# Kernel optimization log

Hardware: AMD Instinct MI355X
Metric: run time of the kernel (lower is better)

Reference implementation:

```python
import jax, jax.numpy as jnp
import numpy as np

# TFMBSLinear forward: quantize input and weight to ternary {-1,0,1} via sign,
# compute out = sign(x) @ sign(W)^T (what the ternary fabric T-GEMV kernel
# computes, with zero-skip), then add float bias. The base-3 byte packing is a
# transport encoding only; the math is the ternary matmul.

def setup_inputs() -> dict:
    key = jax.random.key(0)
    k1, k2, k3 = jax.random.split(key, 3)
    B, IN, OUT = 8192, 2048, 2048
    x = jax.random.normal(k1, (B, IN), dtype=jnp.float32)
    # kaiming-uniform-ish init; only sign matters for the fabric kernel
    weight = jax.random.normal(k2, (OUT, IN), dtype=jnp.float32)
    fan_in_bound = 1.0 / np.sqrt(IN)
    bias = jax.random.uniform(k3, (OUT,), dtype=jnp.float32,
                              minval=-fan_in_bound, maxval=fan_in_bound)
    return {"input": x, "weight": weight, "bias": bias}

def reference(input, weight, bias):
    x_t = jnp.sign(input)    # ternary activations [B, IN]
    w_t = jnp.sign(weight)   # ternary weights     [OUT, IN]
    out = jnp.einsum('bi,oi->bo', x_t, w_t)  # T-GEMV accumulation, fp32
    return out + bias
```

## Files before the change

### kernel.cpp

```cpp
#include <hip/hip_runtime.h>


typedef int   intx4    __attribute__((ext_vector_type(4)));
typedef int   intx8    __attribute__((ext_vector_type(8)));
typedef float floatx16 __attribute__((ext_vector_type(16)));

static constexpr int M = 8192;
static constexpr int N = 2048;
static constexpr int K = 2048;
static constexpr int KB = K / 2;
static constexpr int BM = 128, BN = 128;

__device__ __forceinline__ unsigned nib(float v) {
    unsigned u = __float_as_uint(v);
    return (v != 0.0f) ? (0x2u | ((u >> 28) & 0x8u)) : 0u;
}

__device__ __forceinline__ unsigned pack8(const float4& a, const float4& b) {
    return  nib(a.x)        | (nib(a.y) << 4)  | (nib(a.z) << 8)  | (nib(a.w) << 12)
         | (nib(b.x) << 16) | (nib(b.y) << 20) | (nib(b.z) << 24) | (nib(b.w) << 28);
}

__global__ __launch_bounds__(256) void quant_tile(
    const float* __restrict__ x, const float* __restrict__ w,
    uint4* __restrict__ qx, uint4* __restrict__ qw, int nx, int ntot)
{
    int g = blockIdx.x * 256 + threadIdx.x;
    if (g >= ntot) return;
    const float* src; uint4* dst; int gg;
    if (g < nx) { gg = g; src = x; dst = qx; }
    else        { gg = g - nx; src = w; dst = qw; }
    const int r = gg & 31, h = (gg >> 5) & 1, c = (gg >> 6) & 31, s = gg >> 11;
    const int m = s * 32 + r;
    const float4* p = (const float4*)(src + (size_t)m * K + (c * 2 + h) * 32);
    uint4 o;
    o.x = pack8(p[0], p[1]);
    o.y = pack8(p[2], p[3]);
    o.z = pack8(p[4], p[5]);
    o.w = pack8(p[6], p[7]);
    dst[gg] = o;
}

__device__ __forceinline__ intx8 ext4(intx4 v) {
    return __builtin_shufflevector(v, v, 0, 1, 2, 3, -1, -1, -1, -1);
}

__global__ __launch_bounds__(256, 3) void tgemm_fp4(
    const char* __restrict__ A,
    const char* __restrict__ B,
    const float* __restrict__ bias,
    float* __restrict__ C)
{
    __shared__ char sA[16384];
    __shared__ char sB[16384];

    const int tid  = threadIdx.x;
    const int wave = tid >> 6;
    const int lane = tid & 63;
    const int l32  = lane & 31;
    const int half = lane >> 5;

    const int bm = blockIdx.x * BM;
    const int bn = blockIdx.y * BN;

    const char* gA = A + ((size_t)(bm >> 5) + wave) * 32768 + lane * 16;
    const char* gB = B + ((size_t)(bn >> 5) + wave) * 32768 + lane * 16;
    char* lA = sA + wave * 4096;
    char* lB = sB + wave * 4096;

    const int wm = (wave & 1) * 64;
    const int wn = (wave >> 1) * 64;

    const int aoff = (wm >> 5) * 4096 + lane * 16;
    const int boff = (wn >> 5) * 4096 + lane * 16;

    floatx16 acc[2][2] = {};

    for (int it = 0; it < 8; ++it) {
        const char* ga = gA + it * 4096;
        const char* gb = gB + it * 4096;
        #pragma unroll
        for (int t = 0; t < 4; ++t) {
            __builtin_amdgcn_global_load_lds(
                (const __attribute__((address_space(1))) void*)(ga + t * 1024),
                (__attribute__((address_space(3))) void*)(lA + t * 1024), 16, 0, 0);
            __builtin_amdgcn_global_load_lds(
                (const __attribute__((address_space(1))) void*)(gb + t * 1024),
                (__attribute__((address_space(3))) void*)(lB + t * 1024), 16, 0, 0);
        }
        __syncthreads();

        #pragma unroll
        for (int t = 0; t < 4; ++t) {
            intx4 a0 = *reinterpret_cast<const intx4*>(&sA[aoff          + t * 1024]);
            intx4 a1 = *reinterpret_cast<const intx4*>(&sA[aoff + 4096   + t * 1024]);
            intx4 b0 = *reinterpret_cast<const intx4*>(&sB[boff          + t * 1024]);
            intx4 b1 = *reinterpret_cast<const intx4*>(&sB[boff + 4096   + t * 1024]);
            acc[0][0] = __builtin_amdgcn_mfma_scale_f32_32x32x64_f8f6f4(
                ext4(a0), ext4(b0), acc[0][0], 4, 4, 0, 127, 0, 127);
            acc[0][1] = __builtin_amdgcn_mfma_scale_f32_32x32x64_f8f6f4(
                ext4(a0), ext4(b1), acc[0][1], 4, 4, 0, 127, 0, 127);
            acc[1][0] = __builtin_amdgcn_mfma_scale_f32_32x32x64_f8f6f4(
                ext4(a1), ext4(b0), acc[1][0], 4, 4, 0, 127, 0, 127);
            acc[1][1] = __builtin_amdgcn_mfma_scale_f32_32x32x64_f8f6f4(
                ext4(a1), ext4(b1), acc[1][1], 4, 4, 0, 127, 0, 127);
        }
        __syncthreads();
    }

    const int cn0 = bn + wn + l32;
    const float bc0 = bias[cn0];
    const float bc1 = bias[cn0 + 32];
    const int rbase = bm + wm + 4 * half;

    #pragma unroll
    for (int i = 0; i < 2; ++i) {
        #pragma unroll
        for (int r = 0; r < 16; ++r) {
            const int row = rbase + 32 * i + (r & 3) + 8 * (r >> 2);
            C[(size_t)row * N + cn0]      = acc[i][0][r] + bc0;
            C[(size_t)row * N + cn0 + 32] = acc[i][1][r] + bc1;
        }
    }
}

extern "C" void kernel_launch(void* const* d_in, const int* in_sizes, int n_in,
                              void* d_out, int out_size, void* d_ws, size_t ws_size,
                              hipStream_t stream) {
    const float* x    = (const float*)d_in[0];
    const float* w    = (const float*)d_in[1];
    const float* bias = (const float*)d_in[2];
    float* out = (float*)d_out;

    char* qx = (char*)d_ws;
    char* qw = qx + (size_t)M * KB;

    const int nx   = (M * KB) / 16;
    const int ntot = nx + (N * KB) / 16;
    quant_tile<<<ntot / 256, 256, 0, stream>>>(
        x, w, (uint4*)qx, (uint4*)qw, nx, ntot);

    dim3 grid(M / BM, N / BN);
    tgemm_fp4<<<grid, 256, 0, stream>>>(qx, qw, bias, out);
}
```

Before: 144.6 us.

## Load GEMM operands directly from global into registers, dropping LDS staging

The GEMM kernel no longer stages A/B tiles through shared memory with global_load_lds and barriers. Each wave now reads its fragments straight from global memory (the pre-packed layout already matches the MFMA operand layout), with a 4x-unrolled K loop. It also swaps grid axes so consecutive blocks share the same A rows, raises the occupancy hint to 4 blocks, and writes outputs with nontemporal stores. Removing LDS cuts barriers and LDS traffic, but each tile is now fetched by two waves without sharing, so it relies on L2/cache hit rates and loses latency hiding from staging.

```diff
diff --git a/kernel.cpp b/kernel.cpp
--- a/kernel.cpp
+++ b/kernel.cpp
@@ -10,6 +10,7 @@
 static constexpr int K = 2048;
 static constexpr int KB = K / 2;
 static constexpr int BM = 128, BN = 128;
+
 
 __device__ __forceinline__ unsigned nib(float v) {
     unsigned u = __float_as_uint(v);
@@ -45,67 +46,43 @@
     return __builtin_shufflevector(v, v, 0, 1, 2, 3, -1, -1, -1, -1);
 }
 
-__global__ __launch_bounds__(256, 3) void tgemm_fp4(
+__global__ __launch_bounds__(256, 4) void tgemm_fp4(
     const char* __restrict__ A,
     const char* __restrict__ B,
     const float* __restrict__ bias,
     float* __restrict__ C)
 {
-    __shared__ char sA[16384];
-    __shared__ char sB[16384];
-
     const int tid  = threadIdx.x;
     const int wave = tid >> 6;
     const int lane = tid & 63;
     const int l32  = lane & 31;
     const int half = lane >> 5;
 
-    const int bm = blockIdx.x * BM;
-    const int bn = blockIdx.y * BN;
-
-    const char* gA = A + ((size_t)(bm >> 5) + wave) * 32768 + lane * 16;
-    const char* gB = B + ((size_t)(bn >> 5) + wave) * 32768 + lane * 16;
-    char* lA = sA + wave * 4096;
-    char* lB = sB + wave * 4096;
+    const int bn = blockIdx.x * BN;
+    const int bm = blockIdx.y * BM;
 
     const int wm = (wave & 1) * 64;
     const int wn = (wave >> 1) * 64;
 
-    const int aoff = (wm >> 5) * 4096 + lane * 16;
-    const int boff = (wn >> 5) * 4096 + lane * 16;
+    const char* pa = A + (size_t)((bm + wm) >> 5) * 32768 + lane * 16;
+    const char* pb = B + (size_t)((bn + wn) >> 5) * 32768 + lane * 16;
 
     floatx16 acc[2][2] = {};
 
-    for (int it = 0; it < 8; ++it) {
-        const char* ga = gA + it * 4096;
-        const char* gb = gB + it * 4096;
-        #pragma unroll
-        for (int t = 0; t < 4; ++t) {
-            __builtin_amdgcn_global_load_lds(
-                (const __attribute__((address_space(1))) void*)(ga + t * 1024),
-                (__attribute__((address_space(3))) void*)(lA + t * 1024), 16, 0, 0);
-            __builtin_amdgcn_global_load_lds(
-                (const __attribute__((address_space(1))) void*)(gb + t * 1024),
-                (__attribute__((address_space(3))) void*)(lB + t * 1024), 16, 0, 0);
-        }
-        __syncthreads();
-
-        #pragma unroll
-        for (int t = 0; t < 4; ++t) {
-            intx4 a0 = *reinterpret_cast<const intx4*>(&sA[aoff          + t * 1024]);
-            intx4 a1 = *reinterpret_cast<const intx4*>(&sA[aoff + 4096   + t * 1024]);
-            intx4 b0 = *reinterpret_cast<const intx4*>(&sB[boff          + t * 1024]);
-            intx4 b1 = *reinterpret_cast<const intx4*>(&sB[boff + 4096   + t * 1024]);
-            acc[0][0] = __builtin_amdgcn_mfma_scale_f32_32x32x64_f8f6f4(
-                ext4(a0), ext4(b0), acc[0][0], 4, 4, 0, 127, 0, 127);
-            acc[0][1] = __builtin_amdgcn_mfma_scale_f32_32x32x64_f8f6f4(
-                ext4(a0), ext4(b1), acc[0][1], 4, 4, 0, 127, 0, 127);
-            acc[1][0] = __builtin_amdgcn_mfma_scale_f32_32x32x64_f8f6f4(
-                ext4(a1), ext4(b0), acc[1][0], 4, 4, 0, 127, 0, 127);
-            acc[1][1] = __builtin_amdgcn_mfma_scale_f32_32x32x64_f8f6f4(
-                ext4(a1), ext4(b1), acc[1][1], 4, 4, 0, 127, 0, 127);
-        }
-        __syncthreads();
+    #pragma unroll 4
+    for (int c = 0; c < 32; ++c) {
+        intx4 a0 = *reinterpret_cast<const intx4*>(pa + c * 1024);
+        intx4 a1 = *reinterpret_cast<const intx4*>(pa + 32768 + c * 1024);
+        intx4 b0 = *reinterpret_cast<const intx4*>(pb + c * 1024);
+        intx4 b1 = *reinterpret_cast<const intx4*>(pb + 32768 + c * 1024);
+        acc[0][0] = __builtin_amdgcn_mfma_scale_f32_32x32x64_f8f6f4(
+            ext4(a0), ext4(b0), acc[0][0], 4, 4, 0, 127, 0, 127);
+        acc[0][1] = __builtin_amdgcn_mfma_scale_f32_32x32x64_f8f6f4(
+            ext4(a0), ext4(b1), acc[0][1], 4, 4, 0, 127, 0, 127);
+        acc[1][0] = __builtin_amdgcn_mfma_scale_f32_32x32x64_f8f6f4(
+            ext4(a1), ext4(b0), acc[1][0], 4, 4, 0, 127, 0, 127);
+        acc[1][1] = __builtin_amdgcn_mfma_scale_f32_32x32x64_f8f6f4(
+            ext4(a1), ext4(b1), acc[1][1], 4, 4, 0, 127, 0, 127);
     }
 
     const int cn0 = bn + wn + l32;
@@ -118,8 +95,10 @@
         #pragma unroll
         for (int r = 0; r < 16; ++r) {
             const int row = rbase + 32 * i + (r & 3) + 8 * (r >> 2);
-            C[(size_t)row * N + cn0]      = acc[i][0][r] + bc0;
-            C[(size_t)row * N + cn0 + 32] = acc[i][1][r] + bc1;
+            __builtin_nontemporal_store(acc[i][0][r] + bc0,
+                                        &C[(size_t)row * N + cn0]);
+            __builtin_nontemporal_store(acc[i][1][r] + bc1,
+                                        &C[(size_t)row * N + cn0 + 32]);
         }
     }
 }
@@ -140,6 +119,6 @@
     quant_tile<<<ntot / 256, 256, 0, stream>>>(
         x, w, (uint4*)qx, (uint4*)qw, nx, ntot);
 
-    dim3 grid(M / BM, N / BN);
+    dim3 grid(N / BN, M / BM);
     tgemm_fp4<<<grid, 256, 0, stream>>>(qx, qw, bias, out);
 }
```

After: 151.4 us. 4.7% more time.
